# Performance work log

Measured on AMD Instinct MI355X. Metric: run time of the kernel, lower is better.

Reference implementation:

```python
import jax, jax.numpy as jnp
import numpy as np

# dims
B, T = 256, 64
N_AG, N_FEAT = 10, 4
X_DIM, X_PERM, X_STATIC = 44, 40, 10
HID, XEMB, NHID = 128, 32, 8
E = N_AG * (N_AG - 1)           # 90 directed edges (off-diagonal)
GEMB = NHID * E                 # 720 graph embedding per sample/step
RNN_IN = XEMB + 1 + GEMB        # 753
A_IN = X_STATIC + GEMB          # 730 (x_emb_size2==0 in GraphNN branch)
O_IN = XEMB + X_STATIC + 1 + GEMB  # 763

_off = np.ones((N_AG, N_AG)) - np.eye(N_AG)
RECV = jnp.asarray(np.where(_off)[0])  # rel_rec one-hot == gather by receiver idx
SEND = jnp.asarray(np.where(_off)[1])  # rel_send one-hot == gather by sender idx


def setup_inputs() -> dict:
    key = jax.random.key(0)
    ks = jax.random.split(key, 32)
    w = lambda k, shape: jax.random.normal(k, shape, jnp.float32) * 0.05
    return {
        'x': jax.random.normal(ks[0], (B, T + 1, X_DIM), jnp.float32),
        'x_demo': jax.random.normal(ks[1], (B, X_STATIC), jnp.float32),
        'f_treatment': jax.random.uniform(ks[2], (B, T + 1, 1), jnp.float32),
        'h0': jax.random.normal(ks[3], (B, HID), jnp.float32),
        # x2emb (Linear 4->32), x_static2emb (Linear 10->10)
        'W_x2emb': w(ks[4], (XEMB, X_DIM - X_PERM)), 'b_x2emb': w(ks[5], (XEMB,)),
        'W_stat': w(ks[6], (X_STATIC, X_STATIC)), 'b_stat': w(ks[7], (X_STATIC,)),
        # NRI-style MLP1 (node): 4->8->8 ; MLP2 (edge): 16->8->8
        'W_m1a': w(ks[8], (NHID, N_FEAT)), 'b_m1a': w(ks[9], (NHID,)),
        'W_m1b': w(ks[10], (NHID, NHID)), 'b_m1b': w(ks[11], (NHID,)),
        'W_m2a': w(ks[12], (NHID, 2 * NHID)), 'b_m2a': w(ks[13], (NHID,)),
        'W_m2b': w(ks[14], (NHID, NHID)), 'b_m2b': w(ks[15], (NHID,)),
        # treatment head: Linear(730->128)+ReLU, then Linear(128->1, no bias)
        'W_a1': w(ks[16], (HID, A_IN)), 'b_a1': w(ks[17], (HID,)),
        'W_a2': w(ks[18], (1, HID)),
        # outcome head: Linear(763->128)+ReLU, then Linear(128->1, no bias)
        'W_o1': w(ks[19], (HID, O_IN)), 'b_o1': w(ks[20], (HID,)),
        'W_o2': w(ks[21], (1, HID)),
        # GRUCell(753 -> 128)
        'W_ih': w(ks[22], (3 * HID, RNN_IN)), 'b_ih': w(ks[23], (3 * HID,)),
        'W_hh': w(ks[24], (3 * HID, HID)), 'b_hh': w(ks[25], (3 * HID,)),
    }


def reference(x, x_demo, f_treatment, h0, W_x2emb, b_x2emb, W_stat, b_stat,
              W_m1a, b_m1a, W_m1b, b_m1b, W_m2a, b_m2a, W_m2b, b_m2b,
              W_a1, b_a1, W_a2, W_o1, b_o1, W_o2, W_ih, b_ih, W_hh, b_hh):
    xt = x[:, :T]                       # (B,T,44); len_time = x.size(1)-1
    treat = f_treatment[:, :T]          # (B,T,1)
    demo = x_demo @ W_stat.T + b_stat   # (B,10) static embedding
    demoT = jnp.broadcast_to(demo[:, None], (B, T, X_STATIC))

    # --- GNN(x_permuted): mlp1 per node, node2edge gather, mlp2 per edge ---
    xa = xt[..., :X_PERM].reshape(B, T, N_AG, N_FEAT)
    h1 = jax.nn.elu(xa @ W_m1a.T + b_m1a)
    h1 = jax.nn.elu(h1 @ W_m1b.T + b_m1b)         # (B,T,N_AG,8); BN in eval = identity
    edges = jnp.concatenate([h1[:, :, RECV], h1[:, :, SEND]], axis=-1)  # (B,T,E,16)
    h2 = jax.nn.elu(edges @ W_m2a.T + b_m2a)
    h2 = jax.nn.elu(h2 @ W_m2b.T + b_m2b)         # (B,T,E,8)
    gemb = h2.reshape(B, T, GEMB)                 # (B,T,720)

    xemb = xt[..., X_PERM:] @ W_x2emb.T + b_x2emb  # (B,T,32)

    # --- treatment (a_or_ipw) head; dropout identity in eval ---
    a_in = jnp.concatenate([demoT, gemb], axis=-1)          # (B,T,730)
    a_out = jax.nn.relu(a_in @ W_a1.T + b_a1) @ W_a2.T      # (B,T,1)

    # --- outcome head ---
    o_in = jnp.concatenate([xemb, demoT, treat, gemb], axis=-1)  # (B,T,763)
    y_out = jax.nn.relu(o_in @ W_o1.T + b_o1) @ W_o2.T           # (B,T,1)

    # --- GRUCell recurrence over time ---
    rnn_in = jnp.concatenate([xemb, treat, gemb], axis=-1)  # (B,T,753)
    gi = rnn_in @ W_ih.T + b_ih                             # precompute input proj (B,T,3H)

    def step(h, g):
        gh = h @ W_hh.T + b_hh
        i_r, i_z, i_n = jnp.split(g, 3, axis=-1)
        h_r, h_z, h_n = jnp.split(gh, 3, axis=-1)
        r = jax.nn.sigmoid(i_r + h_r)
        z = jax.nn.sigmoid(i_z + h_z)
        n = jnp.tanh(i_n + r * h_n)
        h_new = (1.0 - z) * n + z * h
        return h_new, h_new

    _, hs = jax.lax.scan(step, h0, jnp.swapaxes(gi, 0, 1))
    hs = jnp.swapaxes(hs, 0, 1)                             # (B,T,128)

    return jnp.concatenate([a_out, y_out, hs], axis=-1)     # (B,T,130)
```

## Files before the change

kernel.cpp:

```cpp
#include <hip/hip_runtime.h>
#include <hip/hip_bf16.h>
#include <math.h>

#define BB     256
#define TT     64
#define BT     (BB*TT)
#define XD     44
#define XP     40
#define XS     10
#define HID    128
#define XEMB   32
#define NHID   8
#define NAG    10
#define NEDGE  90
#define GEMB   720
#define KF     768
#define NTOT   640

typedef __bf16  bf16_t;
typedef __bf16  bf16x8 __attribute__((ext_vector_type(8)));
typedef float   floatx4 __attribute__((ext_vector_type(4)));
typedef _Float16 half2_t __attribute__((ext_vector_type(2)));

__device__ __forceinline__ float elu_f(float v) { return v > 0.f ? v : expm1f(v); }
__device__ __forceinline__ float rcp_fast(float x) { return __builtin_amdgcn_rcpf(x); }
__device__ __forceinline__ float sigmoid_fast(float v) { return rcp_fast(1.f + __expf(-v)); }
__device__ __forceinline__ float tanh_fast(float x) { return 1.f - 2.f * rcp_fast(1.f + __expf(2.f * x)); }

__global__ __launch_bounds__(256) void prep_kernel(
    const float* __restrict__ Wa1, const float* __restrict__ ba1,
    const float* __restrict__ Wo1, const float* __restrict__ bo1,
    const float* __restrict__ Wih, const float* __restrict__ bih,
    bf16_t* __restrict__ WT, float* __restrict__ bcat) {
  int idx = blockIdx.x * 256 + threadIdx.x;
  if (idx >= NTOT * KF) return;
  int n = idx / KF, k = idx - n * KF;
  float v = 0.f;
  if (n < 128) {
    if (k >= 32 && k < 42)        v = Wa1[n * 730 + (k - 32)];
    else if (k >= 43 && k < 763)  v = Wa1[n * 730 + 10 + (k - 43)];
  } else if (n < 256) {
    int m = n - 128;
    if (k < 763)                  v = Wo1[m * 763 + k];
  } else {
    int m = n - 256;
    if (k < 32)                   v = Wih[m * 753 + k];
    else if (k == 42)             v = Wih[m * 753 + 32];
    else if (k >= 43 && k < 763)  v = Wih[m * 753 + 33 + (k - 43)];
  }
  WT[n * KF + k] = (bf16_t)v;
  if (k == 0) {
    bcat[n] = (n < 128) ? ba1[n] : (n < 256 ? bo1[n - 128] : bih[n - 256]);
  }
}

#define W_M1A 0
#define B_M1A 32
#define W_M1B 40
#define B_M1B 104
#define W_M2A 112
#define B_M2A 240
#define W_M2B 248
#define B_M2B 312
#define W_X2E 320
#define B_X2E 448
#define W_ST  480
#define B_ST  580
#define W_TOT 590

__global__ __launch_bounds__(64) void encoder_kernel(
    const float* __restrict__ x, const float* __restrict__ x_demo,
    const float* __restrict__ ftreat,
    const float* __restrict__ Wm1a, const float* __restrict__ bm1a,
    const float* __restrict__ Wm1b, const float* __restrict__ bm1b,
    const float* __restrict__ Wm2a, const float* __restrict__ bm2a,
    const float* __restrict__ Wm2b, const float* __restrict__ bm2b,
    const float* __restrict__ Wx2e, const float* __restrict__ bx2e,
    const float* __restrict__ Wst, const float* __restrict__ bst,
    bf16_t* __restrict__ F) {
  int tok = blockIdx.x;
  int b = tok >> 6, t = tok & 63;
  int tid = threadIdx.x;

  __shared__ float w[W_TOT];
  __shared__ float xl[XD];
  __shared__ float h1a[NAG * 8];
  __shared__ float h1s[NAG * 8];
  __shared__ float h2a[NEDGE * 8];

  for (int i = tid; i < 32;  i += 64) w[W_M1A + i] = Wm1a[i];
  for (int i = tid; i < 8;   i += 64) w[B_M1A + i] = bm1a[i];
  for (int i = tid; i < 64;  i += 64) w[W_M1B + i] = Wm1b[i];
  for (int i = tid; i < 8;   i += 64) w[B_M1B + i] = bm1b[i];
  for (int i = tid; i < 128; i += 64) w[W_M2A + i] = Wm2a[i];
  for (int i = tid; i < 8;   i += 64) w[B_M2A + i] = bm2a[i];
  for (int i = tid; i < 64;  i += 64) w[W_M2B + i] = Wm2b[i];
  for (int i = tid; i < 8;   i += 64) w[B_M2B + i] = bm2b[i];
  for (int i = tid; i < 128; i += 64) w[W_X2E + i] = Wx2e[i];
  for (int i = tid; i < 32;  i += 64) w[B_X2E + i] = bx2e[i];
  for (int i = tid; i < 100; i += 64) w[W_ST + i]  = Wst[i];
  for (int i = tid; i < 10;  i += 64) w[B_ST + i]  = bst[i];
  if (tid < XD) xl[tid] = x[(size_t)(b * 65 + t) * XD + tid];
  __syncthreads();

  for (int c = tid; c < NAG * 8; c += 64) {
    int i = c >> 3, o = c & 7;
    float s = w[B_M1A + o];
#pragma unroll
    for (int f = 0; f < 4; f++) s += xl[i * 4 + f] * w[W_M1A + o * 4 + f];
    h1a[c] = elu_f(s);
  }
  __syncthreads();
  for (int c = tid; c < NAG * 8; c += 64) {
    int i = c >> 3, o = c & 7;
    float s = w[B_M1B + o];
#pragma unroll
    for (int p = 0; p < 8; p++) s += h1a[i * 8 + p] * w[W_M1B + o * 8 + p];
    h1s[c] = elu_f(s);
  }
  __syncthreads();
  for (int c = tid; c < NEDGE * 8; c += 64) {
    int e = c >> 3, o = c & 7;
    int r = e / 9, q = e - 9 * r;
    int sd = q + (q >= r ? 1 : 0);
    float s = w[B_M2A + o];
#pragma unroll
    for (int kk = 0; kk < 8; kk++) s += h1s[r * 8 + kk]  * w[W_M2A + o * 16 + kk];
#pragma unroll
    for (int kk = 0; kk < 8; kk++) s += h1s[sd * 8 + kk] * w[W_M2A + o * 16 + 8 + kk];
    h2a[c] = elu_f(s);
  }
  __syncthreads();

  bf16_t* Frow = F + (size_t)tok * KF;
  for (int c = tid; c < NEDGE * 8; c += 64) {
    int e = c >> 3, o = c & 7;
    float s = w[B_M2B + o];
#pragma unroll
    for (int kk = 0; kk < 8; kk++) s += h2a[e * 8 + kk] * w[W_M2B + o * 8 + kk];
    Frow[43 + c] = (bf16_t)elu_f(s);
  }
  if (tid < 32) {
    float s = w[B_X2E + tid];
#pragma unroll
    for (int f = 0; f < 4; f++) s += xl[40 + f] * w[W_X2E + tid * 4 + f];
    Frow[tid] = (bf16_t)s;
  } else if (tid < 42) {
    int d = tid - 32;
    float s = w[B_ST + d];
#pragma unroll
    for (int j = 0; j < 10; j++) s += x_demo[b * XS + j] * w[W_ST + d * 10 + j];
    Frow[tid] = (bf16_t)s;
  } else if (tid == 42) {
    Frow[42] = (bf16_t)ftreat[b * 65 + t];
  } else if (tid < 48) {
    Frow[720 + tid] = (bf16_t)0.f;
  }
}

__global__ __launch_bounds__(256) void gemm_kernel(
    const bf16_t* __restrict__ F, const bf16_t* __restrict__ WT,
    const float* __restrict__ bcat, float* __restrict__ G) {
  __shared__ __align__(16) bf16_t As[128 * 32];
  __shared__ __align__(16) bf16_t Bs[128 * 32];

  int tid  = threadIdx.x;
  int lane = tid & 63;
  int wv   = tid >> 6;
  int wr   = wv >> 1, wc = wv & 1;
  int m0 = blockIdx.x * 128, n0 = blockIdx.y * 128;

  floatx4 acc[4][4];
#pragma unroll
  for (int i = 0; i < 4; i++)
#pragma unroll
    for (int j = 0; j < 4; j++) acc[i][j] = floatx4{0.f, 0.f, 0.f, 0.f};

  int c0 = tid, c1 = tid + 256;
  int r0 = c0 >> 2, p0 = c0 & 3;
  int r1 = c1 >> 2, p1 = c1 & 3;
  int qr = lane >> 4;
  int lr = lane & 15;

  for (int k0 = 0; k0 < KF; k0 += 32) {
    uint4 a0 = *(const uint4*)(F  + (size_t)(m0 + r0) * KF + k0 + p0 * 8);
    uint4 a1 = *(const uint4*)(F  + (size_t)(m0 + r1) * KF + k0 + p1 * 8);
    uint4 b0 = *(const uint4*)(WT + (size_t)(n0 + r0) * KF + k0 + p0 * 8);
    uint4 b1 = *(const uint4*)(WT + (size_t)(n0 + r1) * KF + k0 + p1 * 8);
    __syncthreads();
    ((uint4*)As)[c0] = a0; ((uint4*)As)[c1] = a1;
    ((uint4*)Bs)[c0] = b0; ((uint4*)Bs)[c1] = b1;
    __syncthreads();

    bf16x8 af[4], bf[4];
#pragma unroll
    for (int i = 0; i < 4; i++) {
      af[i] = *(const bf16x8*)(As + (wr * 64 + i * 16 + lr) * 32 + qr * 8);
      bf[i] = *(const bf16x8*)(Bs + (wc * 64 + i * 16 + lr) * 32 + qr * 8);
    }
#pragma unroll
    for (int i = 0; i < 4; i++)
#pragma unroll
      for (int j = 0; j < 4; j++)
        acc[i][j] = __builtin_amdgcn_mfma_f32_16x16x32_bf16(af[i], bf[j], acc[i][j], 0, 0, 0);
  }

#pragma unroll
  for (int i = 0; i < 4; i++) {
#pragma unroll
    for (int j = 0; j < 4; j++) {
      int col = n0 + wc * 64 + j * 16 + lr;
      float bv = bcat[col];
#pragma unroll
      for (int r = 0; r < 4; r++) {
        int row = m0 + wr * 64 + i * 16 + qr * 4 + r;
        G[(size_t)row * NTOT + col] = acc[i][j][r] + bv;
      }
    }
  }
}

__global__ __launch_bounds__(256) void head_kernel(
    const float* __restrict__ G, const float* __restrict__ Wa2,
    const float* __restrict__ Wo2, float* __restrict__ out) {
  int wid  = (blockIdx.x * 256 + threadIdx.x) >> 6;
  int lane = threadIdx.x & 63;
  const float* g = G + (size_t)wid * NTOT;
  float sa = fmaxf(g[lane], 0.f) * Wa2[lane] + fmaxf(g[lane + 64], 0.f) * Wa2[lane + 64];
  float sy = fmaxf(g[128 + lane], 0.f) * Wo2[lane] + fmaxf(g[192 + lane], 0.f) * Wo2[lane + 64];
#pragma unroll
  for (int off = 32; off > 0; off >>= 1) {
    sa += __shfl_down(sa, off, 64);
    sy += __shfl_down(sy, off, 64);
  }
  if (lane == 0) {
    out[(size_t)wid * 130 + 0] = sa;
    out[(size_t)wid * 130 + 1] = sy;
  }
}

__global__ __launch_bounds__(384, 1) void gru_kernel(
    const float* __restrict__ G, const float* __restrict__ h0,
    const float* __restrict__ Whh, const float* __restrict__ bhh,
    float* __restrict__ out) {
  int b = blockIdx.x;
  int tid = threadIdx.x;
  int lane = tid & 63;
  bool gate = tid < HID;

  __shared__ float gh[384];
  __shared__ unsigned int h2[HID / 2];

  const float* gbase = G + (size_t)b * TT * NTOT;

  half2_t w2[64];
#pragma unroll
  for (int k = 0; k < HID; k += 4) {
    float4 v = *(const float4*)(Whh + (size_t)tid * HID + k);
    w2[k / 2]     = half2_t{(_Float16)v.x, (_Float16)v.y};
    w2[k / 2 + 1] = half2_t{(_Float16)v.z, (_Float16)v.w};
  }
  float bias = bhh[tid];

  float hprev = 0.f, ir = 0.f, iz = 0.f, inn = 0.f;
  if (gate) {
    hprev = h0[(size_t)b * HID + tid];
    ((_Float16*)h2)[tid] = (_Float16)hprev;
    ir  = gbase[256 + tid];
    iz  = gbase[384 + tid];
    inn = gbase[512 + tid];
  }
  __syncthreads();

  for (int t = 0; t < TT; t++) {
    unsigned int hl = h2[lane];
    float nir = 0.f, niz = 0.f, ninn = 0.f;
    if (gate && t + 1 < TT) {
      const float* gn = gbase + (size_t)(t + 1) * NTOT;
      nir  = gn[256 + tid];
      niz  = gn[384 + tid];
      ninn = gn[512 + tid];
    }
    float s0 = 0.f, s1 = 0.f;
#pragma unroll
    for (int k = 0; k < 64; k += 2) {
      int p0 = __builtin_amdgcn_readlane((int)hl, k);
      int p1 = __builtin_amdgcn_readlane((int)hl, k + 1);
      s0 = __builtin_amdgcn_fdot2(w2[k],     __builtin_bit_cast(half2_t, p0), s0, false);
      s1 = __builtin_amdgcn_fdot2(w2[k + 1], __builtin_bit_cast(half2_t, p1), s1, false);
    }
    gh[tid] = s0 + s1 + bias;
    __syncthreads();
    if (gate) {
      float r  = sigmoid_fast(ir + gh[tid]);
      float z  = sigmoid_fast(iz + gh[HID + tid]);
      float nn = tanh_fast(inn + r * gh[2 * HID + tid]);
      float hn = (1.f - z) * nn + z * hprev;
      hprev = hn;
      out[(size_t)(b * TT + t) * 130 + 2 + tid] = hn;
      ((_Float16*)h2)[tid] = (_Float16)hn;
      ir = nir; iz = niz; inn = ninn;
    }
    __syncthreads();
  }
}

extern "C" void kernel_launch(void* const* d_in, const int* in_sizes, int n_in,
                              void* d_out, int out_size, void* d_ws, size_t ws_size,
                              hipStream_t stream) {
  const float* x      = (const float*)d_in[0];
  const float* x_demo = (const float*)d_in[1];
  const float* ftr    = (const float*)d_in[2];
  const float* h0     = (const float*)d_in[3];
  const float* Wx2e   = (const float*)d_in[4];
  const float* bx2e   = (const float*)d_in[5];
  const float* Wst    = (const float*)d_in[6];
  const float* bst    = (const float*)d_in[7];
  const float* Wm1a   = (const float*)d_in[8];
  const float* bm1a   = (const float*)d_in[9];
  const float* Wm1b   = (const float*)d_in[10];
  const float* bm1b   = (const float*)d_in[11];
  const float* Wm2a   = (const float*)d_in[12];
  const float* bm2a   = (const float*)d_in[13];
  const float* Wm2b   = (const float*)d_in[14];
  const float* bm2b   = (const float*)d_in[15];
  const float* Wa1    = (const float*)d_in[16];
  const float* ba1    = (const float*)d_in[17];
  const float* Wa2    = (const float*)d_in[18];
  const float* Wo1    = (const float*)d_in[19];
  const float* bo1    = (const float*)d_in[20];
  const float* Wo2    = (const float*)d_in[21];
  const float* Wih    = (const float*)d_in[22];
  const float* bih    = (const float*)d_in[23];
  const float* Whh    = (const float*)d_in[24];
  const float* bhh    = (const float*)d_in[25];
  float* out = (float*)d_out;

  char* ws = (char*)d_ws;
  bf16_t* F   = (bf16_t*)(ws);
  bf16_t* WT  = (bf16_t*)(ws + 25165824);
  float*  bc  = (float*)(ws + 25165824 + 983040);
  float*  G   = (float*)(ws + 25165824 + 983040 + 2560);

  prep_kernel<<<dim3((NTOT * KF + 255) / 256), dim3(256), 0, stream>>>(
      Wa1, ba1, Wo1, bo1, Wih, bih, WT, bc);
  encoder_kernel<<<dim3(BT), dim3(64), 0, stream>>>(
      x, x_demo, ftr, Wm1a, bm1a, Wm1b, bm1b, Wm2a, bm2a, Wm2b, bm2b,
      Wx2e, bx2e, Wst, bst, F);
  gemm_kernel<<<dim3(BT / 128, NTOT / 128), dim3(256), 0, stream>>>(F, WT, bc, G);
  head_kernel<<<dim3(BT / 4), dim3(256), 0, stream>>>(G, Wa2, Wo2, out);
  gru_kernel<<<dim3(BB), dim3(384), 0, stream>>>(G, h0, Whh, bhh, out);
}
```

Baseline: 242.7 us.

## Batch encoder tokens per block and fuse GRU gates into one thread

```diff
diff --git a/kernel.cpp b/kernel.cpp
--- a/kernel.cpp
+++ b/kernel.cpp
@@ -67,6 +67,7 @@
 #define W_ST  480
 #define B_ST  580
 #define W_TOT 590
+#define TOKS_PER_BLK 8
 
 __global__ __launch_bounds__(64) void encoder_kernel(
     const float* __restrict__ x, const float* __restrict__ x_demo,
@@ -78,11 +79,12 @@
     const float* __restrict__ Wx2e, const float* __restrict__ bx2e,
     const float* __restrict__ Wst, const float* __restrict__ bst,
     bf16_t* __restrict__ F) {
-  int tok = blockIdx.x;
-  int b = tok >> 6, t = tok & 63;
+  int blk = blockIdx.x;
+  int b = blk >> 3, tc = blk & 7;
   int tid = threadIdx.x;
 
   __shared__ float w[W_TOT];
+  __shared__ float demoL[XS];
   __shared__ float xl[XD];
   __shared__ float h1a[NAG * 8];
   __shared__ float h1s[NAG * 8];
@@ -100,61 +102,72 @@
   for (int i = tid; i < 32;  i += 64) w[B_X2E + i] = bx2e[i];
   for (int i = tid; i < 100; i += 64) w[W_ST + i]  = Wst[i];
   for (int i = tid; i < 10;  i += 64) w[B_ST + i]  = bst[i];
-  if (tid < XD) xl[tid] = x[(size_t)(b * 65 + t) * XD + tid];
   __syncthreads();
 
-  for (int c = tid; c < NAG * 8; c += 64) {
-    int i = c >> 3, o = c & 7;
-    float s = w[B_M1A + o];
-#pragma unroll
-    for (int f = 0; f < 4; f++) s += xl[i * 4 + f] * w[W_M1A + o * 4 + f];
-    h1a[c] = elu_f(s);
+  if (tid < 10) {
+    float s = w[B_ST + tid];
+#pragma unroll
+    for (int j = 0; j < 10; j++) s += x_demo[b * XS + j] * w[W_ST + tid * 10 + j];
+    demoL[tid] = s;
   }
   __syncthreads();
-  for (int c = tid; c < NAG * 8; c += 64) {
-    int i = c >> 3, o = c & 7;
-    float s = w[B_M1B + o];
-#pragma unroll
-    for (int p = 0; p < 8; p++) s += h1a[i * 8 + p] * w[W_M1B + o * 8 + p];
-    h1s[c] = elu_f(s);
-  }
-  __syncthreads();
-  for (int c = tid; c < NEDGE * 8; c += 64) {
-    int e = c >> 3, o = c & 7;
-    int r = e / 9, q = e - 9 * r;
-    int sd = q + (q >= r ? 1 : 0);
-    float s = w[B_M2A + o];
-#pragma unroll
-    for (int kk = 0; kk < 8; kk++) s += h1s[r * 8 + kk]  * w[W_M2A + o * 16 + kk];
-#pragma unroll
-    for (int kk = 0; kk < 8; kk++) s += h1s[sd * 8 + kk] * w[W_M2A + o * 16 + 8 + kk];
-    h2a[c] = elu_f(s);
-  }
-  __syncthreads();
-
-  bf16_t* Frow = F + (size_t)tok * KF;
-  for (int c = tid; c < NEDGE * 8; c += 64) {
-    int e = c >> 3, o = c & 7;
-    float s = w[B_M2B + o];
-#pragma unroll
-    for (int kk = 0; kk < 8; kk++) s += h2a[e * 8 + kk] * w[W_M2B + o * 8 + kk];
-    Frow[43 + c] = (bf16_t)elu_f(s);
-  }
-  if (tid < 32) {
-    float s = w[B_X2E + tid];
-#pragma unroll
-    for (int f = 0; f < 4; f++) s += xl[40 + f] * w[W_X2E + tid * 4 + f];
-    Frow[tid] = (bf16_t)s;
-  } else if (tid < 42) {
-    int d = tid - 32;
-    float s = w[B_ST + d];
-#pragma unroll
-    for (int j = 0; j < 10; j++) s += x_demo[b * XS + j] * w[W_ST + d * 10 + j];
-    Frow[tid] = (bf16_t)s;
-  } else if (tid == 42) {
-    Frow[42] = (bf16_t)ftreat[b * 65 + t];
-  } else if (tid < 48) {
-    Frow[720 + tid] = (bf16_t)0.f;
+
+  for (int ti = 0; ti < TOKS_PER_BLK; ti++) {
+    int t = tc * TOKS_PER_BLK + ti;
+    int tok = b * TT + t;
+    if (tid < XD) xl[tid] = x[(size_t)(b * 65 + t) * XD + tid];
+    __syncthreads();
+
+    for (int c = tid; c < NAG * 8; c += 64) {
+      int i = c >> 3, o = c & 7;
+      float s = w[B_M1A + o];
+#pragma unroll
+      for (int f = 0; f < 4; f++) s += xl[i * 4 + f] * w[W_M1A + o * 4 + f];
+      h1a[c] = elu_f(s);
+    }
+    __syncthreads();
+    for (int c = tid; c < NAG * 8; c += 64) {
+      int i = c >> 3, o = c & 7;
+      float s = w[B_M1B + o];
+#pragma unroll
+      for (int p = 0; p < 8; p++) s += h1a[i * 8 + p] * w[W_M1B + o * 8 + p];
+      h1s[c] = elu_f(s);
+    }
+    __syncthreads();
+    for (int c = tid; c < NEDGE * 8; c += 64) {
+      int e = c >> 3, o = c & 7;
+      int r = e / 9, q = e - 9 * r;
+      int sd = q + (q >= r ? 1 : 0);
+      float s = w[B_M2A + o];
+#pragma unroll
+      for (int kk = 0; kk < 8; kk++) s += h1s[r * 8 + kk]  * w[W_M2A + o * 16 + kk];
+#pragma unroll
+      for (int kk = 0; kk < 8; kk++) s += h1s[sd * 8 + kk] * w[W_M2A + o * 16 + 8 + kk];
+      h2a[c] = elu_f(s);
+    }
+    __syncthreads();
+
+    bf16_t* Frow = F + (size_t)tok * KF;
+    for (int c = tid; c < NEDGE * 8; c += 64) {
+      int e = c >> 3, o = c & 7;
+      float s = w[B_M2B + o];
+#pragma unroll
+      for (int kk = 0; kk < 8; kk++) s += h2a[e * 8 + kk] * w[W_M2B + o * 8 + kk];
+      Frow[43 + c] = (bf16_t)elu_f(s);
+    }
+    if (tid < 32) {
+      float s = w[B_X2E + tid];
+#pragma unroll
+      for (int f = 0; f < 4; f++) s += xl[40 + f] * w[W_X2E + tid * 4 + f];
+      Frow[tid] = (bf16_t)s;
+    } else if (tid < 42) {
+      Frow[tid] = (bf16_t)demoL[tid - 32];
+    } else if (tid == 42) {
+      Frow[42] = (bf16_t)ftreat[b * 65 + t];
+    } else if (tid < 48) {
+      Frow[720 + tid] = (bf16_t)0.f;
+    }
+    __syncthreads();
   }
 }
 
@@ -239,69 +252,73 @@
   }
 }
 
-__global__ __launch_bounds__(384, 1) void gru_kernel(
+__global__ __launch_bounds__(128, 2) void gru_kernel(
     const float* __restrict__ G, const float* __restrict__ h0,
     const float* __restrict__ Whh, const float* __restrict__ bhh,
     float* __restrict__ out) {
   int b = blockIdx.x;
   int tid = threadIdx.x;
   int lane = tid & 63;
-  bool gate = tid < HID;
-
-  __shared__ float gh[384];
-  __shared__ unsigned int h2[HID / 2];
+
+  __shared__ unsigned int h2[2][HID / 2];
 
   const float* gbase = G + (size_t)b * TT * NTOT;
 
-  half2_t w2[64];
-#pragma unroll
-  for (int k = 0; k < HID; k += 4) {
-    float4 v = *(const float4*)(Whh + (size_t)tid * HID + k);
-    w2[k / 2]     = half2_t{(_Float16)v.x, (_Float16)v.y};
-    w2[k / 2 + 1] = half2_t{(_Float16)v.z, (_Float16)v.w};
-  }
-  float bias = bhh[tid];
-
-  float hprev = 0.f, ir = 0.f, iz = 0.f, inn = 0.f;
-  if (gate) {
-    hprev = h0[(size_t)b * HID + tid];
-    ((_Float16*)h2)[tid] = (_Float16)hprev;
-    ir  = gbase[256 + tid];
-    iz  = gbase[384 + tid];
-    inn = gbase[512 + tid];
-  }
+  half2_t wr[64], wz[64], wn[64];
+#pragma unroll
+  for (int l = 0; l < 64; l++) {
+    float2 a = *(const float2*)(Whh + (size_t)tid * HID + 2 * l);
+    wr[l] = half2_t{(_Float16)a.x, (_Float16)a.y};
+  }
+#pragma unroll
+  for (int l = 0; l < 64; l++) {
+    float2 a = *(const float2*)(Whh + (size_t)(HID + tid) * HID + 2 * l);
+    wz[l] = half2_t{(_Float16)a.x, (_Float16)a.y};
+  }
+#pragma unroll
+  for (int l = 0; l < 64; l++) {
+    float2 a = *(const float2*)(Whh + (size_t)(2 * HID + tid) * HID + 2 * l);
+    wn[l] = half2_t{(_Float16)a.x, (_Float16)a.y};
+  }
+  float br = bhh[tid], bz = bhh[HID + tid], bn = bhh[2 * HID + tid];
+
+  float hprev = h0[(size_t)b * HID + tid];
+  ((_Float16*)h2[0])[tid] = (_Float16)hprev;
+  float ir = gbase[256 + tid], iz = gbase[384 + tid], inn = gbase[512 + tid];
   __syncthreads();
 
   for (int t = 0; t < TT; t++) {
-    unsigned int hl = h2[lane];
+    unsigned int hl = h2[t & 1][lane];
     float nir = 0.f, niz = 0.f, ninn = 0.f;
-    if (gate && t + 1 < TT) {
+    if (t + 1 < TT) {
       const float* gn = gbase + (size_t)(t + 1) * NTOT;
       nir  = gn[256 + tid];
       niz  = gn[384 + tid];
       ninn = gn[512 + tid];
     }
-    float s0 = 0.f, s1 = 0.f;
-#pragma unroll
-    for (int k = 0; k < 64; k += 2) {
-      int p0 = __builtin_amdgcn_readlane((int)hl, k);
-      int p1 = __builtin_amdgcn_readlane((int)hl, k + 1);
-      s0 = __builtin_amdgcn_fdot2(w2[k],     __builtin_bit_cast(half2_t, p0), s0, false);
-      s1 = __builtin_amdgcn_fdot2(w2[k + 1], __builtin_bit_cast(half2_t, p1), s1, false);
-    }
-    gh[tid] = s0 + s1 + bias;
-    __syncthreads();
-    if (gate) {
-      float r  = sigmoid_fast(ir + gh[tid]);
-      float z  = sigmoid_fast(iz + gh[HID + tid]);
-      float nn = tanh_fast(inn + r * gh[2 * HID + tid]);
-      float hn = (1.f - z) * nn + z * hprev;
-      hprev = hn;
-      out[(size_t)(b * TT + t) * 130 + 2 + tid] = hn;
-      ((_Float16*)h2)[tid] = (_Float16)hn;
-      ir = nir; iz = niz; inn = ninn;
-    }
-    __syncthreads();
+    float sr0 = 0.f, sr1 = 0.f, sz0 = 0.f, sz1 = 0.f, sn0 = 0.f, sn1 = 0.f;
+#pragma unroll
+    for (int l = 0; l < 64; l += 2) {
+      int p0 = __builtin_amdgcn_readlane((int)hl, l);
+      int p1 = __builtin_amdgcn_readlane((int)hl, l + 1);
+      half2_t q0 = __builtin_bit_cast(half2_t, p0);
+      half2_t q1 = __builtin_bit_cast(half2_t, p1);
+      sr0 = __builtin_amdgcn_fdot2(wr[l],     q0, sr0, false);
+      sr1 = __builtin_amdgcn_fdot2(wr[l + 1], q1, sr1, false);
+      sz0 = __builtin_amdgcn_fdot2(wz[l],     q0, sz0, false);
+      sz1 = __builtin_amdgcn_fdot2(wz[l + 1], q1, sz1, false);
+      sn0 = __builtin_amdgcn_fdot2(wn[l],     q0, sn0, false);
+      sn1 = __builtin_amdgcn_fdot2(wn[l + 1], q1, sn1, false);
+    }
+    float r  = sigmoid_fast(ir + sr0 + sr1 + br);
+    float z  = sigmoid_fast(iz + sz0 + sz1 + bz);
+    float nn = tanh_fast(inn + r * (sn0 + sn1 + bn));
+    float hn = (1.f - z) * nn + z * hprev;
+    hprev = hn;
+    ((_Float16*)h2[(t + 1) & 1])[tid] = (_Float16)hn;
+    __syncthreads();
+    out[(size_t)(b * TT + t) * 130 + 2 + tid] = hn;
+    ir = nir; iz = niz; inn = ninn;
   }
 }
 
@@ -344,10 +361,10 @@
 
   prep_kernel<<<dim3((NTOT * KF + 255) / 256), dim3(256), 0, stream>>>(
       Wa1, ba1, Wo1, bo1, Wih, bih, WT, bc);
-  encoder_kernel<<<dim3(BT), dim3(64), 0, stream>>>(
+  encoder_kernel<<<dim3(BT / TOKS_PER_BLK), dim3(64), 0, stream>>>(
       x, x_demo, ftr, Wm1a, bm1a, Wm1b, bm1b, Wm2a, bm2a, Wm2b, bm2b,
       Wx2e, bx2e, Wst, bst, F);
   gemm_kernel<<<dim3(BT / 128, NTOT / 128), dim3(256), 0, stream>>>(F, WT, bc, G);
   head_kernel<<<dim3(BT / 4), dim3(256), 0, stream>>>(G, Wa2, Wo2, out);
-  gru_kernel<<<dim3(BB), dim3(384), 0, stream>>>(G, h0, Whh, bhh, out);
-}
+  gru_kernel<<<dim3(BB), dim3(128), 0, stream>>>(G, h0, Whh, bhh, out);
+}
```

Result: slower. 262.5 us (+8.1%).
